# Kernel optimization log

Hardware: AMD Instinct MI355X
Metric: run time of the kernel (lower is better)

Reference implementation:

```python
import jax, jax.numpy as jnp
import numpy as np

HEAD_NUM = 16
SCALE = 1.0 / np.sqrt(HEAD_NUM)  # source divides by sqrt(head_num), not head_dim
MASK_VAL = -10000000.0


def setup_inputs() -> dict:
    key = jax.random.key(0)
    kq, kk, kv = jax.random.split(key, 3)
    shape = (2, 16, 2048, 64)  # [B, H, L, D]
    Q = jax.random.normal(kq, shape, dtype=jnp.float32)
    K = jax.random.normal(kk, shape, dtype=jnp.float32)
    V = jax.random.normal(kv, shape, dtype=jnp.float32)
    return {"Q": Q, "K": K, "V": V}


def reference(Q, K, V):
    L = Q.shape[-2]
    # [B, H, L, M] attention logits, scaled by 1/sqrt(head_num)
    logits = jnp.einsum('bhld,bhmd->bhlm', Q, K) * SCALE
    # causal mask: strictly-upper triangle gets -1e7 (additive, as in source)
    mask = jnp.triu(jnp.ones((L, L), dtype=logits.dtype), 1) * MASK_VAL
    logits = logits + mask[None, None, :, :]
    weights = jax.nn.softmax(logits, axis=-1)
    return jnp.einsum('bhlm,bhmd->bhld', weights, V)
```

## Files before the change

### kernel.cpp

```cpp
#include <hip/hip_runtime.h>
#include <hip/hip_bf16.h>

#define BM 128
#define BN 64
#define HD 64
#define LQ 2048
#define SD 72

typedef __attribute__((ext_vector_type(8))) short short8;
typedef __attribute__((ext_vector_type(4))) float f32x4;

#define QSCALE 0.360673760222241f

static __device__ __forceinline__ unsigned pk2(float a, float b) {
    union { __hip_bfloat162 h2; unsigned u; } c;
    c.h2 = __float22bfloat162_rn(make_float2(a, b));
    return c.u;
}

__global__ __launch_bounds__(512, 4)
void fa_fwd(const float* __restrict__ Qg,
            const float* __restrict__ Kg,
            const float* __restrict__ Vg,
            float* __restrict__ Og) {
    __shared__ unsigned short sQ[BM][SD];
    __shared__ unsigned short sK[2][BN][SD];
    __shared__ unsigned short sVt[2][HD][SD];
    __shared__ unsigned short sP[8][16][SD];

    const int t    = threadIdx.x;
    const int w    = t >> 6;
    const int lane = t & 63;
    const int qd   = lane >> 4;
    const int l    = lane & 15;

    const int bx  = blockIdx.x;
    const int idx = (bx >> 5) & 7;
    const int qt  = (bx & 256) ? idx : (15 - idx);
    const int bh  = bx & 31;
    const int q0  = qt * BM;

    const size_t base = (size_t)bh * (LQ * HD);
    const float* Qp = Qg + base + (size_t)q0 * HD;
    const float* Kp = Kg + base;
    const float* Vp = Vg + base;

    const int r0 = t >> 4;
    const int c4 = (t & 15) * 4;
    const int RA = w * 4;

#pragma unroll
    for (int p = 0; p < 4; ++p) {
        const int r = p * 32 + r0;
        const float4 v = *(const float4*)(Qp + (size_t)r * HD + c4);
        uint2 u;
        u.x = pk2(v.x * QSCALE, v.y * QSCALE);
        u.y = pk2(v.z * QSCALE, v.w * QSCALE);
        *(uint2*)&sQ[r][c4] = u;
    }

    float4 kA, kB, vA, vB;

    auto issue = [&](int kv0) {
        kA = *(const float4*)(Kp + (size_t)(kv0 + r0) * HD + c4);
        kB = *(const float4*)(Kp + (size_t)(kv0 + 32 + r0) * HD + c4);
        vA = *(const float4*)(Vp + (size_t)(kv0 + RA + qd) * HD + c4);
        vB = *(const float4*)(Vp + (size_t)(kv0 + 32 + RA + qd) * HD + c4);
    };

    auto vstore = [&](float4 vf, int R, int buf) {
        float e0 = vf.x, e1 = vf.y, e2 = vf.z, e3 = vf.w;
        float s0 = (qd & 2) ? e0 : e2;
        float s1 = (qd & 2) ? e1 : e3;
        s0 = __shfl_xor(s0, 32); s1 = __shfl_xor(s1, 32);
        if (qd & 2) { e0 = s0; e1 = s1; } else { e2 = s0; e3 = s1; }
        s0 = (qd & 1) ? e0 : e1;
        s1 = (qd & 1) ? e2 : e3;
        s0 = __shfl_xor(s0, 16); s1 = __shfl_xor(s1, 16);
        if (qd & 1) { e0 = s0; e2 = s1; } else { e1 = s0; e3 = s1; }
        const int d   = c4 + qd;
        const int col = ((((R >> 3) ^ (d >> 3)) & 7) << 3) | (R & 7);
        uint2 u; u.x = pk2(e0, e1); u.y = pk2(e2, e3);
        *(uint2*)&sVt[buf][d][col] = u;
    };

    auto commit = [&](int buf) {
        { uint2 u; u.x = pk2(kA.x, kA.y); u.y = pk2(kA.z, kA.w);
          *(uint2*)&sK[buf][r0][c4] = u; }
        { uint2 u; u.x = pk2(kB.x, kB.y); u.y = pk2(kB.z, kB.w);
          *(uint2*)&sK[buf][32 + r0][c4] = u; }
        vstore(vA, RA, buf);
        vstore(vB, 32 + RA, buf);
    };

    f32x4 accO[4];
#pragma unroll
    for (int mt = 0; mt < 4; ++mt) accO[mt] = (f32x4){0.f, 0.f, 0.f, 0.f};
    float lsum = 0.f;

    const int qrow  = q0 + w * 16 + l;
    const int qminw = q0 + w * 16;
    const int qmaxw = qminw + 15;
    const int n_it  = (q0 + BM) / BN;

    issue(0);
    commit(0);

    for (int it = 0; it < n_it; ++it) {
        const int kv0 = it * BN;
        const int buf = it & 1;
        __syncthreads();
        const bool more = (it + 1 < n_it);
        if (more) issue(kv0 + BN);

        if (kv0 <= qmaxw) {
            f32x4 accS[4];
#pragma unroll
            for (int mt = 0; mt < 4; ++mt) accS[mt] = (f32x4){0.f, 0.f, 0.f, 0.f};
#pragma unroll
            for (int ks = 0; ks < 2; ++ks) {
                const int ko = ks * 32 + qd * 8;
                const short8 bq = *(const short8*)&sQ[w * 16 + l][ko];
#pragma unroll
                for (int mt = 0; mt < 4; ++mt) {
                    const short8 ak = *(const short8*)&sK[buf][mt * 16 + l][ko];
                    accS[mt] = __builtin_amdgcn_mfma_f32_16x16x32_bf16(ak, bq, accS[mt], 0, 0, 0);
                }
            }

            if (kv0 + BN - 1 > qminw) {
#pragma unroll
                for (int mt = 0; mt < 4; ++mt) {
                    const int kvr = kv0 + mt * 16 + qd * 4;
#pragma unroll
                    for (int r = 0; r < 4; ++r)
                        if (kvr + r > qrow) accS[mt][r] = -1e30f;
                }
            }

#pragma unroll
            for (int mt = 0; mt < 4; ++mt) {
#pragma unroll
                for (int r = 0; r < 4; ++r) {
                    const float p = __builtin_amdgcn_exp2f(accS[mt][r]);
                    accS[mt][r] = p;
                    lsum += p;
                }
                uint2 u;
                u.x = pk2(accS[mt][0], accS[mt][1]);
                u.y = pk2(accS[mt][2], accS[mt][3]);
                *(uint2*)&sP[w][l][mt * 16 + qd * 4] = u;
            }
            asm volatile("s_waitcnt lgkmcnt(0)" ::: "memory");

            const int h = l >> 3;
#pragma unroll
            for (int ks = 0; ks < 2; ++ks) {
                const int ko = ks * 32 + qd * 8;
                const short8 bp = *(const short8*)&sP[w][l][ko];
#pragma unroll
                for (int mt = 0; mt < 4; ++mt) {
                    const int row = mt * 16 + l;
                    const int col = (((ks * 4 + qd) ^ (2 * mt + h)) & 7) << 3;
                    const short8 av = *(const short8*)&sVt[buf][row][col];
                    accO[mt] = __builtin_amdgcn_mfma_f32_16x16x32_bf16(av, bp, accO[mt], 0, 0, 0);
                }
            }
        }

        if (more) commit(buf ^ 1);
    }

    lsum += __shfl_xor(lsum, 16);
    lsum += __shfl_xor(lsum, 32);
    const float inv = 1.0f / lsum;
    float* Op = Og + base + (size_t)qrow * HD;
#pragma unroll
    for (int mt = 0; mt < 4; ++mt) {
        float4 o;
        o.x = accO[mt][0] * inv; o.y = accO[mt][1] * inv;
        o.z = accO[mt][2] * inv; o.w = accO[mt][3] * inv;
        *(float4*)(Op + mt * 16 + qd * 4) = o;
    }
}

extern "C" void kernel_launch(void* const* d_in, const int* in_sizes, int n_in,
                              void* d_out, int out_size, void* d_ws, size_t ws_size,
                              hipStream_t stream) {
    const float* Q = (const float*)d_in[0];
    const float* K = (const float*)d_in[1];
    const float* V = (const float*)d_in[2];
    float* O = (float*)d_out;
    fa_fwd<<<dim3(512), dim3(512), 0, stream>>>(Q, K, V, O);
}
```

Measured before the change: 125.9 us.

## Switch to 32x32x16 MFMA with KV-split warps and register-resident P

Reorganizes the attention tile so each warp computes a 32-query by 32-key block using 32x32x16 bf16 MFMA, with four query groups and two key halves per block. Q is held in registers instead of being re-read from LDS, and the P matrix is rearranged with permlane32_swap rather than round-tripping through shared memory. The two key-half partial outputs and row sums are reduced through LDS at the end. This trades an extra final reduction and larger accumulators (register pressure) for fewer LDS reads and fewer, larger MFMA instructions.

```diff
diff --git a/kernel.cpp b/kernel.cpp
--- a/kernel.cpp
+++ b/kernel.cpp
@@ -8,7 +8,7 @@
 #define SD 72
 
 typedef __attribute__((ext_vector_type(8))) short short8;
-typedef __attribute__((ext_vector_type(4))) float f32x4;
+typedef __attribute__((ext_vector_type(16))) float f32x16;
 
 #define QSCALE 0.360673760222241f
 
@@ -23,16 +23,20 @@
             const float* __restrict__ Kg,
             const float* __restrict__ Vg,
             float* __restrict__ Og) {
-    __shared__ unsigned short sQ[BM][SD];
-    __shared__ unsigned short sK[2][BN][SD];
-    __shared__ unsigned short sVt[2][HD][SD];
-    __shared__ unsigned short sP[8][16][SD];
+    __shared__ __align__(16) unsigned short lds[(2 * BN + 2 * HD) * SD];
+    typedef unsigned short KT[BN][SD];
+    typedef unsigned short VT[HD][SD];
+    KT* sK  = (KT*)lds;
+    VT* sVt = (VT*)(lds + 2 * BN * SD);
 
     const int t    = threadIdx.x;
     const int w    = t >> 6;
     const int lane = t & 63;
+    const int h    = lane >> 5;
+    const int l31  = lane & 31;
     const int qd   = lane >> 4;
-    const int l    = lane & 15;
+    const int qg   = w & 3;
+    const int kh   = w >> 2;
 
     const int bx  = blockIdx.x;
     const int idx = (bx >> 5) & 7;
@@ -49,15 +53,27 @@
     const int c4 = (t & 15) * 4;
     const int RA = w * 4;
 
-#pragma unroll
-    for (int p = 0; p < 4; ++p) {
-        const int r = p * 32 + r0;
-        const float4 v = *(const float4*)(Qp + (size_t)r * HD + c4);
-        uint2 u;
-        u.x = pk2(v.x * QSCALE, v.y * QSCALE);
-        u.y = pk2(v.z * QSCALE, v.w * QSCALE);
-        *(uint2*)&sQ[r][c4] = u;
-    }
+    {
+        unsigned short (*sQ)[SD] = (unsigned short (*)[SD])lds;
+#pragma unroll
+        for (int p = 0; p < 4; ++p) {
+            const int r = p * 32 + r0;
+            const float4 v = *(const float4*)(Qp + (size_t)r * HD + c4);
+            uint2 u;
+            u.x = pk2(v.x * QSCALE, v.y * QSCALE);
+            u.y = pk2(v.z * QSCALE, v.w * QSCALE);
+            *(uint2*)&sQ[r][c4] = u;
+        }
+    }
+    __syncthreads();
+    short8 qreg[4];
+    {
+        unsigned short (*sQ)[SD] = (unsigned short (*)[SD])lds;
+#pragma unroll
+        for (int ks = 0; ks < 4; ++ks)
+            qreg[ks] = *(const short8*)&sQ[qg * 32 + l31][ks * 16 + h * 8];
+    }
+    __syncthreads();
 
     float4 kA, kB, vA, vB;
 
@@ -93,14 +109,13 @@
         vstore(vB, 32 + RA, buf);
     };
 
-    f32x4 accO[4];
-#pragma unroll
-    for (int mt = 0; mt < 4; ++mt) accO[mt] = (f32x4){0.f, 0.f, 0.f, 0.f};
+    f32x16 accO[2];
+#pragma unroll
+    for (int r = 0; r < 16; ++r) { accO[0][r] = 0.f; accO[1][r] = 0.f; }
     float lsum = 0.f;
 
-    const int qrow  = q0 + w * 16 + l;
-    const int qminw = q0 + w * 16;
-    const int qmaxw = qminw + 15;
+    const int qminw = q0 + qg * 32;
+    const int qmaxw = qminw + 31;
     const int n_it  = (q0 + BM) / BN;
 
     issue(0);
@@ -113,74 +128,98 @@
         const bool more = (it + 1 < n_it);
         if (more) issue(kv0 + BN);
 
-        if (kv0 <= qmaxw) {
-            f32x4 accS[4];
-#pragma unroll
-            for (int mt = 0; mt < 4; ++mt) accS[mt] = (f32x4){0.f, 0.f, 0.f, 0.f};
-#pragma unroll
-            for (int ks = 0; ks < 2; ++ks) {
-                const int ko = ks * 32 + qd * 8;
-                const short8 bq = *(const short8*)&sQ[w * 16 + l][ko];
-#pragma unroll
-                for (int mt = 0; mt < 4; ++mt) {
-                    const short8 ak = *(const short8*)&sK[buf][mt * 16 + l][ko];
-                    accS[mt] = __builtin_amdgcn_mfma_f32_16x16x32_bf16(ak, bq, accS[mt], 0, 0, 0);
+        if (kv0 + kh * 32 <= qmaxw) {
+            f32x16 accS;
+#pragma unroll
+            for (int r = 0; r < 16; ++r) accS[r] = 0.f;
+#pragma unroll
+            for (int ks = 0; ks < 4; ++ks) {
+                const short8 ak = *(const short8*)&sK[buf][kh * 32 + l31][ks * 16 + h * 8];
+                accS = __builtin_amdgcn_mfma_f32_32x32x16_bf16(ak, qreg[ks], accS, 0, 0, 0);
+            }
+
+            if (kv0 + kh * 32 + 31 > qminw) {
+                const int qrow = qminw + l31;
+                const int kvb  = kv0 + kh * 32 + 4 * h;
+#pragma unroll
+                for (int r = 0; r < 16; ++r) {
+                    const int kv = kvb + (r & 3) + 8 * (r >> 2);
+                    if (kv > qrow) accS[r] = -1e30f;
                 }
             }
 
-            if (kv0 + BN - 1 > qminw) {
-#pragma unroll
-                for (int mt = 0; mt < 4; ++mt) {
-                    const int kvr = kv0 + mt * 16 + qd * 4;
-#pragma unroll
-                    for (int r = 0; r < 4; ++r)
-                        if (kvr + r > qrow) accS[mt][r] = -1e30f;
+#pragma unroll
+            for (int r = 0; r < 16; ++r) {
+                const float p = __builtin_amdgcn_exp2f(accS[r]);
+                accS[r] = p;
+                lsum += p;
+            }
+
+            short8 pf[2];
+#pragma unroll
+            for (int s = 0; s < 2; ++s) {
+                const int rb = s * 8;
+                const unsigned a0 = pk2(accS[rb + 0], accS[rb + 1]);
+                const unsigned b0 = pk2(accS[rb + 4], accS[rb + 5]);
+                const unsigned a1 = pk2(accS[rb + 2], accS[rb + 3]);
+                const unsigned b1 = pk2(accS[rb + 6], accS[rb + 7]);
+                const auto r02 = __builtin_amdgcn_permlane32_swap(a0, b0, 0, 0);
+                const auto r13 = __builtin_amdgcn_permlane32_swap(a1, b1, 0, 0);
+                union { unsigned u[4]; short8 s8; } pu;
+                pu.u[0] = r02[0]; pu.u[1] = r13[0]; pu.u[2] = r02[1]; pu.u[3] = r13[1];
+                pf[s] = pu.s8;
+            }
+
+#pragma unroll
+            for (int s = 0; s < 2; ++s) {
+                const int K0 = kh * 32 + s * 16 + h * 8;
+#pragma unroll
+                for (int dg = 0; dg < 2; ++dg) {
+                    const int d   = dg * 32 + l31;
+                    const int col = (((K0 >> 3) ^ (d >> 3)) & 7) << 3;
+                    const short8 av = *(const short8*)&sVt[buf][d][col];
+                    accO[dg] = __builtin_amdgcn_mfma_f32_32x32x16_bf16(av, pf[s], accO[dg], 0, 0, 0);
                 }
             }
-
-#pragma unroll
-            for (int mt = 0; mt < 4; ++mt) {
-#pragma unroll
-                for (int r = 0; r < 4; ++r) {
-                    const float p = __builtin_amdgcn_exp2f(accS[mt][r]);
-                    accS[mt][r] = p;
-                    lsum += p;
-                }
-                uint2 u;
-                u.x = pk2(accS[mt][0], accS[mt][1]);
-                u.y = pk2(accS[mt][2], accS[mt][3]);
-                *(uint2*)&sP[w][l][mt * 16 + qd * 4] = u;
-            }
-            asm volatile("s_waitcnt lgkmcnt(0)" ::: "memory");
-
-            const int h = l >> 3;
-#pragma unroll
-            for (int ks = 0; ks < 2; ++ks) {
-                const int ko = ks * 32 + qd * 8;
-                const short8 bp = *(const short8*)&sP[w][l][ko];
-#pragma unroll
-                for (int mt = 0; mt < 4; ++mt) {
-                    const int row = mt * 16 + l;
-                    const int col = (((ks * 4 + qd) ^ (2 * mt + h)) & 7) << 3;
-                    const short8 av = *(const short8*)&sVt[buf][row][col];
-                    accO[mt] = __builtin_amdgcn_mfma_f32_16x16x32_bf16(av, bp, accO[mt], 0, 0, 0);
-                }
-            }
         }
 
         if (more) commit(buf ^ 1);
     }
 
-    lsum += __shfl_xor(lsum, 16);
     lsum += __shfl_xor(lsum, 32);
-    const float inv = 1.0f / lsum;
-    float* Op = Og + base + (size_t)qrow * HD;
-#pragma unroll
-    for (int mt = 0; mt < 4; ++mt) {
-        float4 o;
-        o.x = accO[mt][0] * inv; o.y = accO[mt][1] * inv;
-        o.z = accO[mt][2] * inv; o.w = accO[mt][3] * inv;
-        *(float4*)(Op + mt * 16 + qd * 4) = o;
+    __syncthreads();
+    float* fx  = (float*)lds;
+    float* fla = fx + 4 * 64 * 32;
+    if (kh == 1) {
+#pragma unroll
+        for (int dg = 0; dg < 2; ++dg) {
+#pragma unroll
+            for (int r = 0; r < 16; ++r) {
+                const int d = dg * 32 + (r & 3) + 8 * (r >> 2) + 4 * h;
+                fx[(qg * 64 + d) * 32 + l31] = accO[dg][r];
+            }
+        }
+        if (h == 0) fla[qg * 32 + l31] = lsum;
+    }
+    __syncthreads();
+    if (kh == 0) {
+        const float inv  = 1.0f / (lsum + fla[qg * 32 + l31]);
+        const int   qrow = q0 + qg * 32 + l31;
+        float* Op = Og + base + (size_t)qrow * HD;
+#pragma unroll
+        for (int dg = 0; dg < 2; ++dg) {
+#pragma unroll
+            for (int rq = 0; rq < 4; ++rq) {
+                const int d = dg * 32 + 8 * rq + 4 * h;
+                const float* fr = &fx[(qg * 64 + d) * 32 + l31];
+                float4 o;
+                o.x = (accO[dg][rq * 4 + 0] + fr[0])  * inv;
+                o.y = (accO[dg][rq * 4 + 1] + fr[32]) * inv;
+                o.z = (accO[dg][rq * 4 + 2] + fr[64]) * inv;
+                o.w = (accO[dg][rq * 4 + 3] + fr[96]) * inv;
+                *(float4*)(Op + d) = o;
+            }
+        }
     }
 }
 
```

Result: faster. 120.0 us (-4.7%).
